# Kernel tuning notes

Measured on AMD Instinct MI355X. Metric: run time of the kernel, lower is better.

Reference implementation:

```python
import jax, jax.numpy as jnp
import numpy as np

KERNEL_MUL = 2.0
KERNEL_NUM = 5


def _mmd_channel(s, t):
    """Multi-bandwidth Gaussian-kernel MMD for one channel. s,t: [B, D]."""
    B = s.shape[0]
    total = jnp.concatenate([s, t], axis=0)            # [2B, D]
    sq = jnp.sum(total * total, axis=1)                # [2B]
    # ||xi - xj||^2 via Gram identity (avoids [2B,2B,D] intermediate)
    L2 = sq[:, None] + sq[None, :] - 2.0 * (total @ total.T)  # [2B, 2B]
    n = 2 * B
    # torch uses L2_distance.data -> bandwidth is detached
    bandwidth = jax.lax.stop_gradient(jnp.sum(L2)) / (n * n - n)
    bandwidth = bandwidth / (KERNEL_MUL ** (KERNEL_NUM // 2))
    bws = bandwidth * (KERNEL_MUL ** jnp.arange(KERNEL_NUM, dtype=s.dtype))  # [K_num]
    kernels = jnp.sum(jnp.exp(-L2[None, :, :] / bws[:, None, None]), axis=0)  # [2B, 2B]
    XX = kernels[:B, :B]
    YY = kernels[B:, B:]
    XY = kernels[:B, B:]
    YX = kernels[B:, :B]
    return jnp.mean(XX + YY - XY - YX)


def setup_inputs() -> dict:
    key = jax.random.key(0)
    k1, k2 = jax.random.split(key)
    B, K, H, W = 128, 21, 64, 64
    source = jax.random.normal(k1, (B, K, H, W), dtype=jnp.float32)
    target = jax.random.normal(k2, (B, K, H, W), dtype=jnp.float32)
    return {"source": source, "target": target}


def reference(source, target):
    B, K = source.shape[0], source.shape[1]
    s = source.reshape(B, K, -1)  # [B, K, D]
    t = target.reshape(B, K, -1)
    per_channel = jax.vmap(_mmd_channel, in_axes=(1, 1))(s, t)  # [K]
    return jnp.sum(per_channel) / K
```

## Files before the change

### kernel.cpp

```cpp
#include <hip/hip_runtime.h>
#include <hip/hip_bf16.h>
#include <stdint.h>

typedef __attribute__((ext_vector_type(4))) float f32x4;
typedef __attribute__((ext_vector_type(8))) short bf16x8;
typedef __attribute__((ext_vector_type(4))) uint32_t u32x4;

#define NCH 21
#define NROW 256
#define DIM 4096
#define BM 64
#define BK 64
#define LDSS 72
#define NTILE 10

__device__ const int g_TI[NTILE] = {0, 0, 0, 0, 1, 1, 1, 2, 2, 3};
__device__ const int g_TJ[NTILE] = {0, 1, 2, 3, 1, 2, 3, 2, 3, 3};

__device__ __forceinline__ uint32_t pack_bf2(float x, float y) {
  __hip_bfloat162 h = __float22bfloat162_rn(float2{x, y});
  union { __hip_bfloat162 h; uint32_t u; } c;
  c.h = h;
  return c.u;
}

__global__ __launch_bounds__(256) void gram_kernel(
    const float* __restrict__ src, const float* __restrict__ tgt,
    float* __restrict__ Gp, int kshift, int kchunk) {
  const int P = 1 << kshift;
  const int NG = NCH << kshift;
  const int q = NG >> 3, r8 = NG & 7;
  const int x = blockIdx.x & 7;
  const int slot = blockIdx.x >> 3;
  const int cnt = q + (x < r8 ? 1 : 0);
  if (slot >= cnt * NTILE) return;
  const int gbase = (x < r8) ? x * (q + 1) : r8 * (q + 1) + (x - r8) * q;
  const int gi = slot / NTILE;
  const int t = slot - gi * NTILE;
  const int g = gbase + gi;
  const int ch = g >> kshift;
  const int ks = g & (P - 1);
  const int kbase = ks * kchunk;
  const int ti = g_TI[t];
  const int tj = g_TJ[t];
  const bool isdiag = (ti == tj);
  const int tid = threadIdx.x;
  const int lane = tid & 63;

  __shared__ __attribute__((aligned(16))) ushort As[BM * LDSS];
  __shared__ __attribute__((aligned(16))) ushort Bs[BM * LDSS];

  f32x4 acc[2][2];
#pragma unroll
  for (int m = 0; m < 2; ++m)
#pragma unroll
    for (int n = 0; n < 2; ++n)
      acc[m][n] = (f32x4){0.f, 0.f, 0.f, 0.f};

  const int wave = tid >> 6;
  const int wrow = (wave >> 1) * 32;
  const int wcol = (wave & 1) * 32;

  const int r0 = tid >> 3;
  const int c8 = (tid & 7) * 8;
  const float* ap[2];
  const float* bp[2];
#pragma unroll
  for (int p = 0; p < 2; ++p) {
    int ra = ti * BM + r0 + p * 32;
    int rb = tj * BM + r0 + p * 32;
    ap[p] = ((ra < 128) ? src + ((size_t)ra * NCH + ch) * DIM
                        : tgt + ((size_t)(ra - 128) * NCH + ch) * DIM) + c8;
    bp[p] = ((rb < 128) ? src + ((size_t)rb * NCH + ch) * DIM
                        : tgt + ((size_t)(rb - 128) * NCH + ch) * DIM) + c8;
  }

  f32x4 va[2][2], vb[2][2];
#pragma unroll
  for (int p = 0; p < 2; ++p) {
    va[p][0] = *reinterpret_cast<const f32x4*>(ap[p] + kbase);
    va[p][1] = *reinterpret_cast<const f32x4*>(ap[p] + kbase + 4);
    if (!isdiag) {
      vb[p][0] = *reinterpret_cast<const f32x4*>(bp[p] + kbase);
      vb[p][1] = *reinterpret_cast<const f32x4*>(bp[p] + kbase + 4);
    }
  }

  const int kend = kbase + kchunk;
  for (int k0 = kbase; k0 < kend; k0 += BK) {
    __syncthreads();
#pragma unroll
    for (int p = 0; p < 2; ++p) {
      u32x4 wa;
      wa.x = pack_bf2(va[p][0].x, va[p][0].y);
      wa.y = pack_bf2(va[p][0].z, va[p][0].w);
      wa.z = pack_bf2(va[p][1].x, va[p][1].y);
      wa.w = pack_bf2(va[p][1].z, va[p][1].w);
      *reinterpret_cast<u32x4*>(&As[(r0 + p * 32) * LDSS + c8]) = wa;
      if (!isdiag) {
        u32x4 wb;
        wb.x = pack_bf2(vb[p][0].x, vb[p][0].y);
        wb.y = pack_bf2(vb[p][0].z, vb[p][0].w);
        wb.z = pack_bf2(vb[p][1].x, vb[p][1].y);
        wb.w = pack_bf2(vb[p][1].z, vb[p][1].w);
        *reinterpret_cast<u32x4*>(&Bs[(r0 + p * 32) * LDSS + c8]) = wb;
      }
    }
    if (k0 + BK < kend) {
#pragma unroll
      for (int p = 0; p < 2; ++p) {
        va[p][0] = *reinterpret_cast<const f32x4*>(ap[p] + k0 + BK);
        va[p][1] = *reinterpret_cast<const f32x4*>(ap[p] + k0 + BK + 4);
        if (!isdiag) {
          vb[p][0] = *reinterpret_cast<const f32x4*>(bp[p] + k0 + BK);
          vb[p][1] = *reinterpret_cast<const f32x4*>(bp[p] + k0 + BK + 4);
        }
      }
    }
    asm volatile("s_waitcnt lgkmcnt(0)" ::: "memory");
    __builtin_amdgcn_s_barrier();
    asm volatile("" ::: "memory");

    const ushort* Bsrc = isdiag ? As : Bs;
#pragma unroll
    for (int kk = 0; kk < 2; ++kk) {
      const int kb = kk * 32 + (lane >> 4) * 8;
      bf16x8 a[2], b[2];
#pragma unroll
      for (int m = 0; m < 2; ++m)
        a[m] = *reinterpret_cast<const bf16x8*>(
            &As[(wrow + m * 16 + (lane & 15)) * LDSS + kb]);
#pragma unroll
      for (int n = 0; n < 2; ++n)
        b[n] = *reinterpret_cast<const bf16x8*>(
            &Bsrc[(wcol + n * 16 + (lane & 15)) * LDSS + kb]);
#pragma unroll
      for (int m = 0; m < 2; ++m)
#pragma unroll
        for (int n = 0; n < 2; ++n)
          acc[m][n] = __builtin_amdgcn_mfma_f32_16x16x32_bf16(a[m], b[n],
                                                              acc[m][n], 0, 0, 0);
    }
  }

  float* gp = Gp + (size_t)(ch * P + ks) * (NROW * NROW);
  const int rbase = ti * BM + wrow + ((lane >> 4) << 2);
  const int cbase = tj * BM + wcol + (lane & 15);
#pragma unroll
  for (int m = 0; m < 2; ++m)
#pragma unroll
    for (int n = 0; n < 2; ++n)
#pragma unroll
      for (int j = 0; j < 4; ++j)
        gp[(size_t)(rbase + m * 16 + j) * NROW + (cbase + n * 16)] = acc[m][n][j];
}

__device__ __forceinline__ float block_sum256(float v, float* sm) {
#pragma unroll
  for (int o = 32; o > 0; o >>= 1) v += __shfl_down(v, o, 64);
  const int lane = threadIdx.x & 63;
  const int w = threadIdx.x >> 6;
  if (lane == 0) sm[w] = v;
  __syncthreads();
  float r = 0.f;
  if (threadIdx.x == 0) r = sm[0] + sm[1] + sm[2] + sm[3];
  __syncthreads();
  return r;
}

__global__ __launch_bounds__(256) void foldsum_kernel(
    const f32x4* __restrict__ Gp, f32x4* __restrict__ Gf,
    float* __restrict__ sums, int P) {
  const int t = blockIdx.x;
  const int ch = blockIdx.y;
  const int ti = g_TI[t], tj = g_TJ[t];
  const bool isdiag = (ti == tj);
  const int tid = threadIdx.x;
  float s = 0.f, tr = 0.f;
#pragma unroll
  for (int i = 0; i < 4; ++i) {
    const int idx4 = tid * 4 + i;
    const int rrow = idx4 >> 4;
    const int c4 = idx4 & 15;
    const int base_v = (ti * 64 + rrow) * 64 + tj * 16 + c4;
    f32x4 v = Gp[(size_t)(ch * P) * 16384 + base_v];
    for (int p = 1; p < P; ++p) v += Gp[(size_t)(ch * P + p) * 16384 + base_v];
    Gf[(size_t)ch * 16384 + base_v] = v;
    s += (v.x + v.y) + (v.z + v.w);
    if (isdiag) {
      const int cb = c4 * 4;
#pragma unroll
      for (int e = 0; e < 4; ++e)
        if (cb + e == rrow) tr += v[e];
    }
  }
  __shared__ float sm[4];
  float sG = block_sum256(s, sm);
  float sT = block_sum256(tr, sm);
  if (tid == 0) {
    sums[ch * 20 + t] = sG;
    if (isdiag) sums[ch * 20 + 10 + ti] = sT;
  }
}

__global__ __launch_bounds__(256) void mmd_kernel(const float* __restrict__ Gf,
                                                  const float* __restrict__ sums,
                                                  float* __restrict__ partial) {
  const int t = blockIdx.x;
  const int ch = blockIdx.y;
  const int ti = g_TI[t], tj = g_TJ[t];
  const int tid = threadIdx.x;
  const float* g = Gf + (size_t)ch * (NROW * NROW);

  const float* sc = sums + ch * 20;
  float sumG = 0.f;
#pragma unroll
  for (int k = 0; k < NTILE; ++k)
    sumG += (g_TI[k] == g_TJ[k] ? 1.f : 2.f) * sc[k];
  const float trace = (sc[10] + sc[11]) + (sc[12] + sc[13]);
  const float sumL2 = 2.f * NROW * trace - 2.f * sumG;
  const float bw = sumL2 / (float)(NROW * NROW - NROW) * 0.25f;
  float inv[5];
#pragma unroll
  for (int a = 0; a < 5; ++a) inv[a] = -1.f / (bw * (float)(1 << a));

  __shared__ float dA[64], dB[64];
  if (tid < 64) dA[tid] = g[(size_t)(ti * 64 + tid) * (NROW + 1)];
  else if (tid < 128) dB[tid - 64] = g[(size_t)(tj * 64 + (tid - 64)) * (NROW + 1)];
  __syncthreads();

  const int col = tid & 63;
  const int qq = tid >> 6;
  const float dj = dB[col];
  float acc = 0.f;
#pragma unroll 4
  for (int it = 0; it < 16; ++it) {
    const int r = it * 4 + qq;
    const float L2 = dA[r] + dj - 2.f * g[(size_t)(ti * 64 + r) * NROW + tj * 64 + col];
    float kv = 0.f;
#pragma unroll
    for (int a = 0; a < 5; ++a) kv += __expf(L2 * inv[a]);
    acc += kv;
  }
  __shared__ float sm[4];
  float tot = block_sum256(acc, sm);
  if (tid == 0) {
    float w = (ti == tj) ? 1.f : 2.f;
    float sgn = ((ti >= 2) == (tj >= 2)) ? 1.f : -1.f;
    partial[ch * NTILE + t] = tot * w * sgn;
  }
}

__global__ __launch_bounds__(256) void final_kernel(const float* __restrict__ partial,
                                                    float* __restrict__ out) {
  const int tid = threadIdx.x;
  float v = (tid < NCH * NTILE) ? partial[tid] : 0.f;
  __shared__ float sm[4];
  float tot = block_sum256(v, sm);
  if (tid == 0) out[0] = tot * (1.f / (NCH * 128.f * 128.f));
}

extern "C" void kernel_launch(void* const* d_in, const int* in_sizes, int n_in,
                              void* d_out, int out_size, void* d_ws, size_t ws_size,
                              hipStream_t stream) {
  const float* src = (const float*)d_in[0];
  const float* tgt = (const float*)d_in[1];
  float* out = (float*)d_out;
  const size_t GSZ = (size_t)NROW * NROW;

  int kshift = 0;
  if (ws_size >= (NCH * 9 * GSZ + 512) * sizeof(float)) kshift = 3;
  else if (ws_size >= (NCH * 5 * GSZ + 512) * sizeof(float)) kshift = 2;
  else if (ws_size >= (NCH * 3 * GSZ + 512) * sizeof(float)) kshift = 1;
  const int P = 1 << kshift;

  float* Gp = (float*)d_ws;
  float* Gf = (P > 1) ? Gp + (size_t)NCH * P * GSZ : Gp;
  float* sums = Gf + (size_t)NCH * GSZ;
  float* partial = sums + NCH * 20;

  const int NG = NCH * P;
  const int q = NG / 8, r8 = NG % 8;
  const int grid = 8 * (q + (r8 ? 1 : 0)) * NTILE;

  gram_kernel<<<dim3(grid), 256, 0, stream>>>(src, tgt, Gp, kshift, DIM >> kshift);
  foldsum_kernel<<<dim3(NTILE, NCH), 256, 0, stream>>>((const f32x4*)Gp,
                                                       (f32x4*)Gf, sums, P);
  mmd_kernel<<<dim3(NTILE, NCH), 256, 0, stream>>>(Gf, sums, partial);
  final_kernel<<<1, 256, 0, stream>>>(partial, out);
}
```

Baseline: 47.42 us.

## Enlarge Gram tiles to 128x128 blocks with 512 threads per block

After: 45.91 us. 3.2% less time.

```diff
diff --git a/kernel.cpp b/kernel.cpp
--- a/kernel.cpp
+++ b/kernel.cpp
@@ -9,7 +9,7 @@
 #define NCH 21
 #define NROW 256
 #define DIM 4096
-#define BM 64
+#define BMP 128
 #define BK 64
 #define LDSS 72
 #define NTILE 10
@@ -24,7 +24,7 @@
   return c.u;
 }
 
-__global__ __launch_bounds__(256) void gram_kernel(
+__global__ __launch_bounds__(512) void gram_kernel(
     const float* __restrict__ src, const float* __restrict__ tgt,
     float* __restrict__ Gp, int kshift, int kchunk) {
   const int P = 1 << kshift;
@@ -33,46 +33,44 @@
   const int x = blockIdx.x & 7;
   const int slot = blockIdx.x >> 3;
   const int cnt = q + (x < r8 ? 1 : 0);
-  if (slot >= cnt * NTILE) return;
+  if (slot >= cnt * 3) return;
   const int gbase = (x < r8) ? x * (q + 1) : r8 * (q + 1) + (x - r8) * q;
-  const int gi = slot / NTILE;
-  const int t = slot - gi * NTILE;
+  const int gi = slot / 3;
+  const int bt = slot - gi * 3;
   const int g = gbase + gi;
   const int ch = g >> kshift;
   const int ks = g & (P - 1);
   const int kbase = ks * kchunk;
-  const int ti = g_TI[t];
-  const int tj = g_TJ[t];
-  const bool isdiag = (ti == tj);
+  const int row_base = (bt == 1) ? 128 : 0;
+  const int col_base = (bt == 0) ? 0 : 128;
+  const bool isdiag = (bt != 2);
   const int tid = threadIdx.x;
   const int lane = tid & 63;
 
-  __shared__ __attribute__((aligned(16))) ushort As[BM * LDSS];
-  __shared__ __attribute__((aligned(16))) ushort Bs[BM * LDSS];
-
-  f32x4 acc[2][2];
+  __shared__ __attribute__((aligned(16))) ushort As[BMP * LDSS];
+  __shared__ __attribute__((aligned(16))) ushort Bs[BMP * LDSS];
+
+  f32x4 acc[2][4];
 #pragma unroll
   for (int m = 0; m < 2; ++m)
 #pragma unroll
-    for (int n = 0; n < 2; ++n)
+    for (int n = 0; n < 4; ++n)
       acc[m][n] = (f32x4){0.f, 0.f, 0.f, 0.f};
 
   const int wave = tid >> 6;
-  const int wrow = (wave >> 1) * 32;
-  const int wcol = (wave & 1) * 32;
+  const int wr = (wave >> 1) * 32;
+  const int wc = (wave & 1) * 64;
 
   const int r0 = tid >> 3;
   const int c8 = (tid & 7) * 8;
+  const float* Ab = row_base ? tgt : src;
+  const float* Bb = col_base ? tgt : src;
   const float* ap[2];
   const float* bp[2];
 #pragma unroll
   for (int p = 0; p < 2; ++p) {
-    int ra = ti * BM + r0 + p * 32;
-    int rb = tj * BM + r0 + p * 32;
-    ap[p] = ((ra < 128) ? src + ((size_t)ra * NCH + ch) * DIM
-                        : tgt + ((size_t)(ra - 128) * NCH + ch) * DIM) + c8;
-    bp[p] = ((rb < 128) ? src + ((size_t)rb * NCH + ch) * DIM
-                        : tgt + ((size_t)(rb - 128) * NCH + ch) * DIM) + c8;
+    ap[p] = Ab + ((size_t)(r0 + p * 64) * NCH + ch) * DIM + c8;
+    bp[p] = Bb + ((size_t)(r0 + p * 64) * NCH + ch) * DIM + c8;
   }
 
   f32x4 va[2][2], vb[2][2];
@@ -96,14 +94,14 @@
       wa.y = pack_bf2(va[p][0].z, va[p][0].w);
       wa.z = pack_bf2(va[p][1].x, va[p][1].y);
       wa.w = pack_bf2(va[p][1].z, va[p][1].w);
-      *reinterpret_cast<u32x4*>(&As[(r0 + p * 32) * LDSS + c8]) = wa;
+      *reinterpret_cast<u32x4*>(&As[(r0 + p * 64) * LDSS + c8]) = wa;
       if (!isdiag) {
         u32x4 wb;
         wb.x = pack_bf2(vb[p][0].x, vb[p][0].y);
         wb.y = pack_bf2(vb[p][0].z, vb[p][0].w);
         wb.z = pack_bf2(vb[p][1].x, vb[p][1].y);
         wb.w = pack_bf2(vb[p][1].z, vb[p][1].w);
-        *reinterpret_cast<u32x4*>(&Bs[(r0 + p * 32) * LDSS + c8]) = wb;
+        *reinterpret_cast<u32x4*>(&Bs[(r0 + p * 64) * LDSS + c8]) = wb;
       }
     }
     if (k0 + BK < kend) {
@@ -125,34 +123,36 @@
 #pragma unroll
     for (int kk = 0; kk < 2; ++kk) {
       const int kb = kk * 32 + (lane >> 4) * 8;
-      bf16x8 a[2], b[2];
+      bf16x8 a[2], b[4];
 #pragma unroll
       for (int m = 0; m < 2; ++m)
         a[m] = *reinterpret_cast<const bf16x8*>(
-            &As[(wrow + m * 16 + (lane & 15)) * LDSS + kb]);
-#pragma unroll
-      for (int n = 0; n < 2; ++n)
+            &As[(wr + m * 16 + (lane & 15)) * LDSS + kb]);
+#pragma unroll
+      for (int n = 0; n < 4; ++n)
         b[n] = *reinterpret_cast<const bf16x8*>(
-            &Bsrc[(wcol + n * 16 + (lane & 15)) * LDSS + kb]);
+            &Bsrc[(wc + n * 16 + (lane & 15)) * LDSS + kb]);
 #pragma unroll
       for (int m = 0; m < 2; ++m)
 #pragma unroll
-        for (int n = 0; n < 2; ++n)
+        for (int n = 0; n < 4; ++n)
           acc[m][n] = __builtin_amdgcn_mfma_f32_16x16x32_bf16(a[m], b[n],
                                                               acc[m][n], 0, 0, 0);
     }
   }
 
   float* gp = Gp + (size_t)(ch * P + ks) * (NROW * NROW);
-  const int rbase = ti * BM + wrow + ((lane >> 4) << 2);
-  const int cbase = tj * BM + wcol + (lane & 15);
 #pragma unroll
   for (int m = 0; m < 2; ++m)
 #pragma unroll
-    for (int n = 0; n < 2; ++n)
+    for (int n = 0; n < 4; ++n) {
+      const int grow = row_base + wr + m * 16 + ((lane >> 4) << 2);
+      const int gcol = col_base + wc + n * 16 + (lane & 15);
+      if ((grow >> 6) > (gcol >> 6)) continue;
 #pragma unroll
       for (int j = 0; j < 4; ++j)
-        gp[(size_t)(rbase + m * 16 + j) * NROW + (cbase + n * 16)] = acc[m][n][j];
+        gp[(size_t)(grow + j) * NROW + gcol] = acc[m][n][j];
+    }
 }
 
 __device__ __forceinline__ float block_sum256(float v, float* sm) {
@@ -281,9 +281,9 @@
 
   const int NG = NCH * P;
   const int q = NG / 8, r8 = NG % 8;
-  const int grid = 8 * (q + (r8 ? 1 : 0)) * NTILE;
-
-  gram_kernel<<<dim3(grid), 256, 0, stream>>>(src, tgt, Gp, kshift, DIM >> kshift);
+  const int grid = 8 * (q + (r8 ? 1 : 0)) * 3;
+
+  gram_kernel<<<dim3(grid), 512, 0, stream>>>(src, tgt, Gp, kshift, DIM >> kshift);
   foldsum_kernel<<<dim3(NTILE, NCH), 256, 0, stream>>>((const f32x4*)Gp,
                                                        (f32x4*)Gf, sums, P);
   mmd_kernel<<<dim3(NTILE, NCH), 256, 0, stream>>>(Gf, sums, partial);
```
